# Kernel tuning notes

Hardware: AMD Instinct MI355X
Metric: run time of the kernel (lower is better)

Reference implementation:

```python
import jax, jax.numpy as jnp
import numpy as np

NUM_CARDS = 71
NUM_SLOTS = 71
TRUMP_DIM = 7
HIDDEN = [512, 256, 128]
ACTIONS = 9
BATCH = 16384


def setup_inputs() -> dict:
    key = jax.random.key(0)
    ks = jax.random.split(key, 16)
    state_idx = jax.random.randint(ks[0], (BATCH, NUM_SLOTS), 0, NUM_CARDS, dtype=jnp.int32)
    trump_onehot = jax.random.uniform(ks[1], (BATCH, TRUMP_DIM), dtype=jnp.float32)
    legal_mask = jnp.ones((BATCH, ACTIONS), dtype=bool)
    in_dim = NUM_SLOTS * NUM_CARDS + TRUMP_DIM  # 5048
    dims = [in_dim] + HIDDEN
    params = {}
    for i, (d_in, d_out) in enumerate(zip(dims[:-1], dims[1:])):
        params[f"W{i}"] = jax.random.normal(ks[2 + 2 * i], (d_in, d_out), dtype=jnp.float32) * 0.02
        params[f"b{i}"] = jnp.zeros((d_out,), dtype=jnp.float32)
    params["Wp"] = jax.random.normal(ks[10], (dims[-1], ACTIONS), dtype=jnp.float32) * 0.02
    params["bp"] = jnp.zeros((ACTIONS,), dtype=jnp.float32)
    return {"state_idx": state_idx, "trump_onehot": trump_onehot, "legal_mask": legal_mask, **params}


def reference(state_idx, trump_onehot, legal_mask,
              W0, b0, W1, b1, W2, b2, Wp, bp):
    # one-hot encode 71 card slots and flatten: (B, 71*71)
    idx = jnp.clip(state_idx, 0, NUM_CARDS - 1)
    one_hot = jax.nn.one_hot(idx, NUM_CARDS, dtype=jnp.float32)
    flat = one_hot.reshape(one_hot.shape[0], -1)
    x = jnp.concatenate([flat, trump_onehot], axis=1)  # (B, 5048)
    x = jax.nn.relu(x @ W0 + b0)
    x = jax.nn.relu(x @ W1 + b1)
    x = jax.nn.relu(x @ W2 + b2)
    logits = x @ Wp + bp  # (B, 9)
    logits = jnp.where(legal_mask, logits, -jnp.inf)
    return jax.nn.log_softmax(logits, axis=1)
```

## Files before the change

### kernel.cpp

```cpp
#include <hip/hip_runtime.h>
#include <hip/hip_bf16.h>

typedef unsigned int u32;
typedef unsigned short u16;
typedef unsigned char u8;
typedef _Float16 f16;
typedef __attribute__((ext_vector_type(2)))  _Float16 f16x2;
typedef __attribute__((ext_vector_type(8)))  _Float16 f16x8;
typedef __attribute__((ext_vector_type(16))) _Float16 f16x16;
typedef __attribute__((ext_vector_type(4))) float f32x4;

#define NSLOT   71
#define NCARD   71
#define ONEHOT  5041
#define INDIM   5048
#define D0      512
#define D1      256
#define D2      128
#define NACT    9

__device__ __forceinline__ u16 f2h_bits(float x) { f16 h = (f16)x; u16 r; __builtin_memcpy(&r, &h, 2); return r; }

__global__ void prep_kernel(const float* __restrict__ W0, const float* __restrict__ W1,
                            const float* __restrict__ W2,
                            u16* __restrict__ W0h, u16* __restrict__ W1T, u16* __restrict__ W2T) {
    int i = blockIdx.x * 256 + threadIdx.x;
    const int q0 = (INDIM * D0) / 4;
    const int n1 = D0 * D1;
    const int n2 = D1 * D2;
    if (i < q0) {
        float4 w = ((const float4*)W0)[i];
        ushort4 o;
        o.x = f2h_bits(w.x); o.y = f2h_bits(w.y);
        o.z = f2h_bits(w.z); o.w = f2h_bits(w.w);
        ((ushort4*)W0h)[i] = o;
    } else if (i < q0 + n1) {
        int j = i - q0; int n = j >> 9, k = j & 511;
        W1T[j] = f2h_bits(W1[k * D1 + n]);
    } else if (i < q0 + n1 + n2) {
        int j = i - q0 - n1; int n = j >> 8, k = j & 255;
        W2T[j] = f2h_bits(W2[k * D2 + n]);
    }
}

__global__ __launch_bounds__(512)
void layer0_kernel(const int* __restrict__ sidx, const float* __restrict__ trump,
                   const float* __restrict__ b0, const u16* __restrict__ W0h,
                   u16* __restrict__ h0) {
    __shared__ u8 idxl[128 * NSLOT];
    __shared__ float trl[128 * 7];
    const int tid = threadIdx.x;
    const int ct = blockIdx.x & 3;
    const int rbase = (blockIdx.x >> 2) * 128;

    for (int i = tid; i < 128 * NSLOT; i += 512) {
        int v = sidx[rbase * NSLOT + i];
        v = v < 0 ? 0 : (v > NCARD - 1 ? NCARD - 1 : v);
        idxl[i] = (u8)v;
    }
    for (int i = tid; i < 128 * 7; i += 512)
        trl[i] = trump[rbase * 7 + i];
    __syncthreads();

    const int rg = tid >> 3;
    const int cg = tid & 7;
    const int c0 = ct * 128 + cg * 16;
    const u8* ix0 = &idxl[(rg * 2 + 0) * NSLOT];
    const u8* ix1 = &idxl[(rg * 2 + 1) * NSLOT];
    const u16* Wc = W0h + c0;

    f16x16 acc0, acc1;
    {
        f16x16 bias;
        #pragma unroll
        for (int j = 0; j < 16; ++j) bias[j] = (f16)b0[c0 + j];
        acc0 = bias; acc1 = bias;
        #pragma unroll
        for (int t = 0; t < 7; ++t) {
            f16x16 w16 = *(const f16x16*)(Wc + (size_t)(ONEHOT + t) * D0);
            acc0 += w16 * (f16)trl[(rg * 2 + 0) * 7 + t];
            acc1 += w16 * (f16)trl[(rg * 2 + 1) * 7 + t];
        }
    }

#define LD0(s) (*(const f16x16*)(Wc + ((size_t)(s) * NCARD + ix0[(s)]) * D0))
#define LD1(s) (*(const f16x16*)(Wc + ((size_t)(s) * NCARD + ix1[(s)]) * D0))

    f16x16 pa0 = LD0(0), pa1 = LD1(0);
    f16x16 pb0 = LD0(1), pb1 = LD1(1);
    int s = 0;
    for (; s + 3 < NSLOT; s += 2) {
        f16x16 na0 = LD0(s + 2), na1 = LD1(s + 2);
        f16x16 nb0 = LD0(s + 3), nb1 = LD1(s + 3);
        __builtin_amdgcn_sched_barrier(0);
        acc0 += pa0; acc1 += pa1;
        acc0 += pb0; acc1 += pb1;
        pa0 = na0; pa1 = na1; pb0 = nb0; pb1 = nb1;
    }
    {
        f16x16 nc0 = LD0(70), nc1 = LD1(70);
        __builtin_amdgcn_sched_barrier(0);
        acc0 += pa0; acc1 += pa1;
        acc0 += pb0; acc1 += pb1;
        acc0 += nc0; acc1 += nc1;
    }
#undef LD0
#undef LD1

    const f16x16 zero = {};
    f16x16 v0 = __builtin_elementwise_max(acc0, zero);
    f16x16 v1 = __builtin_elementwise_max(acc1, zero);
    uint4* dst0 = (uint4*)(h0 + (size_t)(rbase + rg * 2 + 0) * D0 + c0);
    uint4* dst1 = (uint4*)(h0 + (size_t)(rbase + rg * 2 + 1) * D0 + c0);
    dst0[0] = ((const uint4*)&v0)[0];
    dst0[1] = ((const uint4*)&v0)[1];
    dst1[0] = ((const uint4*)&v1)[0];
    dst1[1] = ((const uint4*)&v1)[1];
}

__global__ __launch_bounds__(512)
void mlp_kernel(const u16* __restrict__ h0, const u16* __restrict__ W1T, const u16* __restrict__ W2T,
                const float* __restrict__ b1, const float* __restrict__ b2,
                const float* __restrict__ Wp, const float* __restrict__ bp,
                const int* __restrict__ legal, float* __restrict__ out) {
    __shared__ __align__(16) u16 Abuf[32 * 520];
    __shared__ u16 h1buf[32 * 264];
    __shared__ u16 h2buf[32 * 136];
    __shared__ float wpb[D2 * NACT + NACT];
    const int tid = threadIdx.x;
    const int r0 = blockIdx.x * 32;
    const int wv = tid >> 6;
    const int ln = tid & 63;

    #pragma unroll
    for (int k = 0; k < 4; ++k) {
        int r = wv + k * 8;
        const u32* gp = (const u32*)(h0 + (size_t)(r0 + r) * D0 + ln * 8);
        u32* lp = (u32*)&Abuf[r * 520];
        __builtin_amdgcn_global_load_lds((const __attribute__((address_space(1))) u32*)gp,
                                         (__attribute__((address_space(3))) u32*)lp,
                                         16, 0, 0);
    }
    for (int i = tid; i < D2 * NACT + NACT; i += 512)
        wpb[i] = (i < D2 * NACT) ? Wp[i] : bp[i - D2 * NACT];
    __syncthreads();

    const int w  = wv;
    const int l  = ln;
    const int lc = l & 15;
    const int kg = l >> 4;

    {
        const int n0 = w * 32;
        f32x4 a00 = {0.f,0.f,0.f,0.f}, a01 = a00, a10 = a00, a11 = a00;
        for (int kb = 0; kb < D0; kb += 32) {
            f16x8 av0 = *(const f16x8*)&Abuf[lc * 520 + kb + kg * 8];
            f16x8 av1 = *(const f16x8*)&Abuf[(lc + 16) * 520 + kb + kg * 8];
            f16x8 bv0 = *(const f16x8*)(W1T + (size_t)(n0 + lc) * D0 + kb + kg * 8);
            f16x8 bv1 = *(const f16x8*)(W1T + (size_t)(n0 + 16 + lc) * D0 + kb + kg * 8);
            a00 = __builtin_amdgcn_mfma_f32_16x16x32_f16(av0, bv0, a00, 0, 0, 0);
            a01 = __builtin_amdgcn_mfma_f32_16x16x32_f16(av0, bv1, a01, 0, 0, 0);
            a10 = __builtin_amdgcn_mfma_f32_16x16x32_f16(av1, bv0, a10, 0, 0, 0);
            a11 = __builtin_amdgcn_mfma_f32_16x16x32_f16(av1, bv1, a11, 0, 0, 0);
        }
        #pragma unroll
        for (int nb = 0; nb < 2; ++nb) {
            int col = n0 + nb * 16 + lc;
            float bias = b1[col];
            #pragma unroll
            for (int j = 0; j < 4; ++j) {
                f32x4 v0 = nb ? a01 : a00;
                f32x4 v1 = nb ? a11 : a10;
                h1buf[(kg * 4 + j) * 264 + col]        = f2h_bits(fmaxf(v0[j] + bias, 0.f));
                h1buf[(16 + kg * 4 + j) * 264 + col]   = f2h_bits(fmaxf(v1[j] + bias, 0.f));
            }
        }
    }
    __syncthreads();

    {
        const int n0 = w * 16;
        f32x4 c0 = {0.f,0.f,0.f,0.f}, c1 = c0;
        for (int kb = 0; kb < D1; kb += 32) {
            f16x8 av0 = *(const f16x8*)&h1buf[lc * 264 + kb + kg * 8];
            f16x8 av1 = *(const f16x8*)&h1buf[(lc + 16) * 264 + kb + kg * 8];
            f16x8 bv  = *(const f16x8*)(W2T + (size_t)(n0 + lc) * D1 + kb + kg * 8);
            c0 = __builtin_amdgcn_mfma_f32_16x16x32_f16(av0, bv, c0, 0, 0, 0);
            c1 = __builtin_amdgcn_mfma_f32_16x16x32_f16(av1, bv, c1, 0, 0, 0);
        }
        int col = n0 + lc;
        float bias = b2[col];
        #pragma unroll
        for (int j = 0; j < 4; ++j) {
            h2buf[(kg * 4 + j) * 136 + col]      = f2h_bits(fmaxf(c0[j] + bias, 0.f));
            h2buf[(16 + kg * 4 + j) * 136 + col] = f2h_bits(fmaxf(c1[j] + bias, 0.f));
        }
    }
    __syncthreads();

    if (tid < 128) {
        int r = tid >> 2, q = tid & 3;
        float part[NACT];
        #pragma unroll
        for (int a = 0; a < NACT; ++a) part[a] = 0.f;
        int kbase = q * 32;
        #pragma unroll
        for (int kk = 0; kk < 32; kk += 2) {
            u32 pr = *(const u32*)&h2buf[r * 136 + kbase + kk];
            f16x2 hp; __builtin_memcpy(&hp, &pr, 4);
            float x0 = (float)hp.x, x1 = (float)hp.y;
            #pragma unroll
            for (int a = 0; a < NACT; ++a)
                part[a] += x0 * wpb[(kbase + kk) * NACT + a] + x1 * wpb[(kbase + kk + 1) * NACT + a];
        }
        #pragma unroll
        for (int a = 0; a < NACT; ++a) {
            part[a] += __shfl_xor(part[a], 1, 64);
            part[a] += __shfl_xor(part[a], 2, 64);
        }
        if (q == 0) {
            int row = r0 + r;
            const int* mk = legal + (size_t)row * NACT;
            float lg[NACT]; float mx = -INFINITY;
            #pragma unroll
            for (int a = 0; a < NACT; ++a) {
                lg[a] = part[a] + wpb[D2 * NACT + a];
                if (mk[a] != 0 && lg[a] > mx) mx = lg[a];
            }
            float s = 0.f;
            #pragma unroll
            for (int a = 0; a < NACT; ++a) if (mk[a] != 0) s += __expf(lg[a] - mx);
            float lse = mx + __logf(s);
            #pragma unroll
            for (int a = 0; a < NACT; ++a)
                out[(size_t)row * NACT + a] = (mk[a] != 0) ? (lg[a] - lse) : -INFINITY;
        }
    }
}

extern "C" void kernel_launch(void* const* d_in, const int* in_sizes, int n_in,
                              void* d_out, int out_size, void* d_ws, size_t ws_size,
                              hipStream_t stream) {
    const int*   sidx  = (const int*)d_in[0];
    const float* trump = (const float*)d_in[1];
    const int*   legal = (const int*)d_in[2];
    const float* W0 = (const float*)d_in[3];
    const float* b0 = (const float*)d_in[4];
    const float* W1 = (const float*)d_in[5];
    const float* b1 = (const float*)d_in[6];
    const float* W2 = (const float*)d_in[7];
    const float* b2 = (const float*)d_in[8];
    const float* Wp = (const float*)d_in[9];
    const float* bp = (const float*)d_in[10];
    float* out = (float*)d_out;

    u16* W0h  = (u16*)d_ws;
    u16* W1T  = W0h + (size_t)INDIM * D0;
    u16* W2T  = W1T + (size_t)D0 * D1;
    u16* h0   = W2T + (size_t)D1 * D2;

    const int nprep = (INDIM * D0) / 4 + D0 * D1 + D1 * D2;
    prep_kernel<<<(nprep + 255) / 256, 256, 0, stream>>>(W0, W1, W2, W0h, W1T, W2T);
    layer0_kernel<<<512, 512, 0, stream>>>(sidx, trump, b0, W0h, h0);
    mlp_kernel<<<512, 512, 0, stream>>>(h0, W1T, W2T, b1, b2, Wp, bp, legal, out);
}
```

Baseline: 82.81 us.

## Drop weight prep kernel; gather fp32 W0 directly and fold W1/W2 transposes into layer0

Removes the separate prep kernel that converted the whole 5048x512 W0 to fp16. Layer0 now gathers fp32 rows of W0 directly and accumulates in fp32. The W1/W2 transpose-to-fp16 work moves into the first threads of layer0_kernel, which saves a kernel launch and a full pass over W0. In exchange each gather reads twice as many bytes and holds twice as many accumulator registers, which may lower occupancy or bandwidth efficiency.

```diff
diff --git a/kernel.cpp b/kernel.cpp
--- a/kernel.cpp
+++ b/kernel.cpp
@@ -8,7 +8,8 @@
 typedef __attribute__((ext_vector_type(2)))  _Float16 f16x2;
 typedef __attribute__((ext_vector_type(8)))  _Float16 f16x8;
 typedef __attribute__((ext_vector_type(16))) _Float16 f16x16;
-typedef __attribute__((ext_vector_type(4))) float f32x4;
+typedef __attribute__((ext_vector_type(4)))  float f32x4;
+typedef __attribute__((ext_vector_type(16))) float f32x16;
 
 #define NSLOT   71
 #define NCARD   71
@@ -21,31 +22,11 @@
 
 __device__ __forceinline__ u16 f2h_bits(float x) { f16 h = (f16)x; u16 r; __builtin_memcpy(&r, &h, 2); return r; }
 
-__global__ void prep_kernel(const float* __restrict__ W0, const float* __restrict__ W1,
-                            const float* __restrict__ W2,
-                            u16* __restrict__ W0h, u16* __restrict__ W1T, u16* __restrict__ W2T) {
-    int i = blockIdx.x * 256 + threadIdx.x;
-    const int q0 = (INDIM * D0) / 4;
-    const int n1 = D0 * D1;
-    const int n2 = D1 * D2;
-    if (i < q0) {
-        float4 w = ((const float4*)W0)[i];
-        ushort4 o;
-        o.x = f2h_bits(w.x); o.y = f2h_bits(w.y);
-        o.z = f2h_bits(w.z); o.w = f2h_bits(w.w);
-        ((ushort4*)W0h)[i] = o;
-    } else if (i < q0 + n1) {
-        int j = i - q0; int n = j >> 9, k = j & 511;
-        W1T[j] = f2h_bits(W1[k * D1 + n]);
-    } else if (i < q0 + n1 + n2) {
-        int j = i - q0 - n1; int n = j >> 8, k = j & 255;
-        W2T[j] = f2h_bits(W2[k * D2 + n]);
-    }
-}
-
 __global__ __launch_bounds__(512)
 void layer0_kernel(const int* __restrict__ sidx, const float* __restrict__ trump,
-                   const float* __restrict__ b0, const u16* __restrict__ W0h,
+                   const float* __restrict__ b0, const float* __restrict__ W0,
+                   const float* __restrict__ W1, const float* __restrict__ W2,
+                   u16* __restrict__ W1T, u16* __restrict__ W2T,
                    u16* __restrict__ h0) {
     __shared__ u8 idxl[128 * NSLOT];
     __shared__ float trl[128 * 7];
@@ -53,6 +34,19 @@
     const int ct = blockIdx.x & 3;
     const int rbase = (blockIdx.x >> 2) * 128;
 
+    {
+        int gid = blockIdx.x * 512 + tid;
+        const int n1 = D0 * D1;
+        const int n2 = D1 * D2;
+        if (gid < n1) {
+            int n = gid >> 9, k = gid & 511;
+            W1T[gid] = f2h_bits(W1[k * D1 + n]);
+        } else if (gid < n1 + n2) {
+            int j = gid - n1; int n = j >> 8, k = j & 255;
+            W2T[j] = f2h_bits(W2[k * D2 + n]);
+        }
+    }
+
     for (int i = tid; i < 128 * NSLOT; i += 512) {
         int v = sidx[rbase * NSLOT + i];
         v = v < 0 ? 0 : (v > NCARD - 1 ? NCARD - 1 : v);
@@ -67,38 +61,36 @@
     const int c0 = ct * 128 + cg * 16;
     const u8* ix0 = &idxl[(rg * 2 + 0) * NSLOT];
     const u8* ix1 = &idxl[(rg * 2 + 1) * NSLOT];
-    const u16* Wc = W0h + c0;
-
-    f16x16 acc0, acc1;
-    {
-        f16x16 bias;
-        #pragma unroll
-        for (int j = 0; j < 16; ++j) bias[j] = (f16)b0[c0 + j];
+    const float* Wc = W0 + c0;
+
+    f32x16 acc0, acc1;
+    {
+        f32x16 bias = *(const f32x16*)(b0 + c0);
         acc0 = bias; acc1 = bias;
         #pragma unroll
         for (int t = 0; t < 7; ++t) {
-            f16x16 w16 = *(const f16x16*)(Wc + (size_t)(ONEHOT + t) * D0);
-            acc0 += w16 * (f16)trl[(rg * 2 + 0) * 7 + t];
-            acc1 += w16 * (f16)trl[(rg * 2 + 1) * 7 + t];
-        }
-    }
-
-#define LD0(s) (*(const f16x16*)(Wc + ((size_t)(s) * NCARD + ix0[(s)]) * D0))
-#define LD1(s) (*(const f16x16*)(Wc + ((size_t)(s) * NCARD + ix1[(s)]) * D0))
-
-    f16x16 pa0 = LD0(0), pa1 = LD1(0);
-    f16x16 pb0 = LD0(1), pb1 = LD1(1);
+            f32x16 w = *(const f32x16*)(Wc + (size_t)(ONEHOT + t) * D0);
+            acc0 += w * trl[(rg * 2 + 0) * 7 + t];
+            acc1 += w * trl[(rg * 2 + 1) * 7 + t];
+        }
+    }
+
+#define LD0(s) (*(const f32x16*)(Wc + ((size_t)(s) * NCARD + ix0[(s)]) * D0))
+#define LD1(s) (*(const f32x16*)(Wc + ((size_t)(s) * NCARD + ix1[(s)]) * D0))
+
+    f32x16 pa0 = LD0(0), pa1 = LD1(0);
+    f32x16 pb0 = LD0(1), pb1 = LD1(1);
     int s = 0;
     for (; s + 3 < NSLOT; s += 2) {
-        f16x16 na0 = LD0(s + 2), na1 = LD1(s + 2);
-        f16x16 nb0 = LD0(s + 3), nb1 = LD1(s + 3);
+        f32x16 na0 = LD0(s + 2), na1 = LD1(s + 2);
+        f32x16 nb0 = LD0(s + 3), nb1 = LD1(s + 3);
         __builtin_amdgcn_sched_barrier(0);
         acc0 += pa0; acc1 += pa1;
         acc0 += pb0; acc1 += pb1;
         pa0 = na0; pa1 = na1; pb0 = nb0; pb1 = nb1;
     }
     {
-        f16x16 nc0 = LD0(70), nc1 = LD1(70);
+        f32x16 nc0 = LD0(70), nc1 = LD1(70);
         __builtin_amdgcn_sched_barrier(0);
         acc0 += pa0; acc1 += pa1;
         acc0 += pb0; acc1 += pb1;
@@ -107,15 +99,18 @@
 #undef LD0
 #undef LD1
 
-    const f16x16 zero = {};
-    f16x16 v0 = __builtin_elementwise_max(acc0, zero);
-    f16x16 v1 = __builtin_elementwise_max(acc1, zero);
+    u16 o0[16], o1[16];
+    #pragma unroll
+    for (int j = 0; j < 16; ++j) {
+        o0[j] = f2h_bits(fmaxf(acc0[j], 0.f));
+        o1[j] = f2h_bits(fmaxf(acc1[j], 0.f));
+    }
     uint4* dst0 = (uint4*)(h0 + (size_t)(rbase + rg * 2 + 0) * D0 + c0);
     uint4* dst1 = (uint4*)(h0 + (size_t)(rbase + rg * 2 + 1) * D0 + c0);
-    dst0[0] = ((const uint4*)&v0)[0];
-    dst0[1] = ((const uint4*)&v0)[1];
-    dst1[0] = ((const uint4*)&v1)[0];
-    dst1[1] = ((const uint4*)&v1)[1];
+    dst0[0] = ((const uint4*)o0)[0];
+    dst0[1] = ((const uint4*)o0)[1];
+    dst1[0] = ((const uint4*)o1)[0];
+    dst1[1] = ((const uint4*)o1)[1];
 }
 
 __global__ __launch_bounds__(512)
@@ -254,13 +249,10 @@
     const float* bp = (const float*)d_in[10];
     float* out = (float*)d_out;
 
-    u16* W0h  = (u16*)d_ws;
-    u16* W1T  = W0h + (size_t)INDIM * D0;
+    u16* W1T  = (u16*)d_ws;
     u16* W2T  = W1T + (size_t)D0 * D1;
     u16* h0   = W2T + (size_t)D1 * D2;
 
-    const int nprep = (INDIM * D0) / 4 + D0 * D1 + D1 * D2;
-    prep_kernel<<<(nprep + 255) / 256, 256, 0, stream>>>(W0, W1, W2, W0h, W1T, W2T);
-    layer0_kernel<<<512, 512, 0, stream>>>(sidx, trump, b0, W0h, h0);
+    layer0_kernel<<<512, 512, 0, stream>>>(sidx, trump, b0, W0, W1, W2, W1T, W2T, h0);
     mlp_kernel<<<512, 512, 0, stream>>>(h0, W1T, W2T, b1, b2, Wp, bp, legal, out);
 }
```

Measured after the change: 171.6 us. +107.2%, slower.
